# Optimization experiments

Hardware: AMD Instinct MI355X
Metric: run time of the kernel (lower is better)

## Reference

```python
import jax, jax.numpy as jnp
import numpy as np

B, S, H, E = 8, 512, 1024, 8
T = B * S            # total tokens
CAP = T // E         # capacity, capacity_factor = 1.0


def _moe(x, wg, ew1, eb1, ew2, eb2):
    # x: [T, H] tokens; top-1 gating with capacity, DeepSpeed-style dispatch/combine
    gates = jax.nn.softmax(x @ wg)                      # [T, E]
    idx = jnp.argmax(gates, axis=-1)                    # [T]
    mask1 = jax.nn.one_hot(idx, E, dtype=x.dtype)       # [T, E]
    locations = jnp.cumsum(mask1, axis=0) - 1.0         # position within expert queue
    mask1 = mask1 * (locations < CAP).astype(x.dtype)   # drop overflow tokens
    gates1 = jnp.sum(gates * mask1, axis=-1)            # [T] combine weight
    locs = jnp.sum(locations * mask1, axis=-1).astype(jnp.int32)  # [T]
    loc_oh = jax.nn.one_hot(locs, CAP, dtype=x.dtype)   # [T, C]
    combine = gates1[:, None, None] * mask1[:, :, None] * loc_oh[:, None, :]  # [T,E,C]
    dispatch = (combine > 0).astype(x.dtype)            # [T, E, C]
    xd = jnp.einsum('sec,sm->ecm', dispatch, x)         # gather tokens per expert
    h = jnp.einsum('ecm,emn->ecn', xd, ew1) + eb1[:, None, :]
    h = jnp.einsum('ecn,enp->ecp', h, ew2) + eb2[:, None, :]
    return jnp.einsum('sec,ecm->sm', combine, h)        # scatter back, weighted


def setup_inputs() -> dict:
    key = jax.random.key(0)
    ks = jax.random.split(key, 16)
    w = lambda k, shape: jax.random.normal(k, shape, jnp.float32) * 0.02
    return {
        'x': jax.random.normal(ks[0], (B, S, H), jnp.float32),
        'y': jax.random.randint(ks[1], (B,), 0, H),
        'w1': w(ks[2], (H, H)), 'b1': jnp.zeros((H,), jnp.float32),
        'w2': w(ks[3], (H, H)), 'b2': jnp.zeros((H,), jnp.float32),
        'w3': w(ks[4], (H, H)), 'b3': jnp.zeros((H,), jnp.float32),
        'wg1': w(ks[5], (H, E)),
        'e1_w1': w(ks[6], (E, H, H)), 'e1_b1': jnp.zeros((E, H), jnp.float32),
        'e1_w2': w(ks[7], (E, H, H)), 'e1_b2': jnp.zeros((E, H), jnp.float32),
        'wg2': w(ks[8], (H, E)),
        'e2_w1': w(ks[9], (E, H, H)), 'e2_b1': jnp.zeros((E, H), jnp.float32),
        'e2_w2': w(ks[10], (E, H, H)), 'e2_b2': jnp.zeros((E, H), jnp.float32),
    }


def reference(x, y, w1, b1, w2, b2, w3, b3, wg1, e1_w1, e1_b1, e1_w2, e1_b2,
              wg2, e2_w1, e2_b1, e2_w2, e2_b2):
    xf = x.reshape(-1, H)                               # [T, H]
    hidden = xf @ w1 + b1
    out = _moe(hidden, wg1, e1_w1, e1_b1, e1_w2, e1_b2)
    out = out @ w2 + b2
    out = _moe(out, wg2, e2_w1, e2_b1, e2_w2, e2_b2)
    out = out @ w3 + b3
    hidden = hidden + out
    sent = hidden.reshape(B, S, H).mean(axis=1)         # [B, H] logits
    logp = jax.nn.log_softmax(sent, axis=-1)
    return -jnp.mean(logp[jnp.arange(B), y])
```

## Files before the change

kernel.cpp:

```cpp
#include <hip/hip_runtime.h>

#define TOK 4096
#define HID 1024
#define NEXP 8
#define CAP 512
#define WSZ 1048576

typedef _Float16 f16;
typedef f16 f16x8 __attribute__((ext_vector_type(8)));
typedef f16 f16x4 __attribute__((ext_vector_type(4)));
typedef f16 f16x2 __attribute__((ext_vector_type(2)));
typedef float f32x4 __attribute__((ext_vector_type(4)));

typedef const __attribute__((address_space(1))) void gvoid;
typedef __attribute__((address_space(3))) void lvoid;

__device__ __forceinline__ void gld16(const void* g, void* l) {
  __builtin_amdgcn_global_load_lds((gvoid*)g, (lvoid*)l, 16, 0, 0);
}

__device__ __forceinline__ void wtrans(const float* __restrict__ src,
                                       f16* __restrict__ dst,
                                       int nb, int kb0, float* lds, int tid)
{
  const int n = tid >> 3, seg = tid & 7;
  #define WSTAGE(ks, buf)                                                    \
    {                                                                        \
      _Pragma("unroll")                                                      \
      for (int i = 0; i < 2; ++i) {                                          \
        int p = i * 512 + tid;                                               \
        int r = p >> 4, c = p & 15;                                          \
        int cg = c ^ ((r >> 2) & 15);                                        \
        gld16(src + (size_t)(kb0 + (ks) * 64 + r) * HID + nb + cg * 4,       \
              lds + (buf) * 4096 + p * 4);                                   \
      }                                                                      \
    }
  WSTAGE(0, 0);
  #pragma unroll
  for (int s = 0; s < 4; ++s) {
    if (s == 0)      { WSTAGE(1, 1); asm volatile("s_waitcnt vmcnt(2)" ::: "memory"); }
    else if (s == 1) { WSTAGE(2, 0); asm volatile("s_waitcnt vmcnt(3)" ::: "memory"); }
    else if (s == 2) { WSTAGE(3, 1); asm volatile("s_waitcnt vmcnt(3)" ::: "memory"); }
    else             {               asm volatile("s_waitcnt vmcnt(1)" ::: "memory"); }
    asm volatile("s_barrier" ::: "memory");
    const float* B = lds + (s & 1) * 4096;
    f16x8 o;
    #pragma unroll
    for (int j = 0; j < 8; ++j) {
      int r = seg * 8 + j;
      int cl = (n >> 2) ^ ((r >> 2) & 15);
      o[j] = (f16)B[r * 64 + cl * 4 + (n & 3)];
    }
    *(f16x8*)&dst[(size_t)(nb + n) * HID + kb0 + s * 64 + seg * 8] = o;
    asm volatile("s_barrier" ::: "memory");
  }
  #undef WSTAGE
}

template<int MODE>
__global__ __launch_bounds__(512, 4) void gemm_fused(
    const f16* __restrict__ A, const f16* __restrict__ Bt,
    const float* __restrict__ bias, f16* __restrict__ C,
    const int* __restrict__ rowmap, const float* __restrict__ gmax,
    int rowsPerExpert, long bStride, int biasStride,
    const float* __restrict__ tsrc, f16* __restrict__ tdst, int nGemm)
{
  __shared__ __align__(16) unsigned char smem[65536];
  const int tid = threadIdx.x;

  if ((int)blockIdx.x >= nGemm) {
    const int tb = blockIdx.x - nGemm;
    const int mat = tb >> 6, slab = tb & 63;
    wtrans(tsrc + (size_t)mat * WSZ, tdst + (size_t)mat * WSZ,
           (slab & 15) * 64, (slab >> 4) * 256, (float*)smem, tid);
    return;
  }

  f16* As0 = (f16*)smem;
  f16* Bs0 = (f16*)(smem + 32768);
  const int w = tid >> 6, l = tid & 63;
  const int wr = w >> 2, wc = w & 3;

  const int orig = blockIdx.x;
  const int sw = (orig & 7) * 32 + (orig >> 3);
  const int bx = sw & 7, by = sw >> 3;
  const int e = (by * 128) / rowsPerExpert;

  const int lr = l >> 3;
  const int chunkSw = ((l & 7) ^ lr) * 8;

  const f16* pst[4];
  if (w < 4) {
    #pragma unroll
    for (int i = 0; i < 4; ++i) {
      int r = by * 128 + w * 32 + i * 8 + lr;
      long tok = r;
      if (MODE == 1) { int t = rowmap[r]; tok = (t < 0) ? (long)TOK : (long)t; }
      pst[i] = A + tok * HID + chunkSw;
    }
  } else {
    #pragma unroll
    for (int i = 0; i < 4; ++i)
      pst[i] = Bt + (size_t)e * bStride
             + (size_t)(bx * 128 + (w - 4) * 32 + i * 8 + lr) * HID + chunkSw;
  }

  f32x4 acc[4][2];
  #pragma unroll
  for (int i = 0; i < 4; ++i)
    #pragma unroll
    for (int j = 0; j < 2; ++j) acc[i][j] = (f32x4){0.f, 0.f, 0.f, 0.f};

  const int g = l >> 4, c = l & 15, sa = c & 7;

  {
    f16* db = (w < 4) ? As0 + (w * 32) * 64 : Bs0 + ((w - 4) * 32) * 64;
    #pragma unroll
    for (int i = 0; i < 4; ++i) gld16(pst[i], db + i * 8 * 64);
  }

  int cur = 0;
  for (int t = 0; t < 15; ++t) {
    {
      const int k0 = (t + 1) * 64;
      f16* db = (w < 4) ? As0 + ((cur ^ 1) * 8192) + (w * 32) * 64
                        : Bs0 + ((cur ^ 1) * 8192) + ((w - 4) * 32) * 64;
      #pragma unroll
      for (int i = 0; i < 4; ++i) gld16(pst[i] + k0, db + i * 8 * 64);
    }
    asm volatile("s_waitcnt vmcnt(4)" ::: "memory");
    asm volatile("s_barrier" ::: "memory");
    __builtin_amdgcn_s_setprio(1);
    #pragma unroll
    for (int h = 0; h < 2; ++h) {
      const int q = ((h * 4 + g) ^ sa) * 8;
      f16x8 af[4], bf[2];
      #pragma unroll
      for (int mi = 0; mi < 4; ++mi)
        af[mi] = *(const f16x8*)&As0[cur * 8192 + (wr * 64 + mi * 16 + c) * 64 + q];
      #pragma unroll
      for (int ni = 0; ni < 2; ++ni)
        bf[ni] = *(const f16x8*)&Bs0[cur * 8192 + (wc * 32 + ni * 16 + c) * 64 + q];
      #pragma unroll
      for (int mi = 0; mi < 4; ++mi)
        #pragma unroll
        for (int ni = 0; ni < 2; ++ni)
          acc[mi][ni] = __builtin_amdgcn_mfma_f32_16x16x32_f16(
              af[mi], bf[ni], acc[mi][ni], 0, 0, 0);
    }
    __builtin_amdgcn_s_setprio(0);
    asm volatile("s_barrier" ::: "memory");
    cur ^= 1;
  }
  asm volatile("s_waitcnt vmcnt(0)" ::: "memory");
  asm volatile("s_barrier" ::: "memory");
  __builtin_amdgcn_s_setprio(1);
  #pragma unroll
  for (int h = 0; h < 2; ++h) {
    const int q = ((h * 4 + g) ^ sa) * 8;
    f16x8 af[4], bf[2];
    #pragma unroll
    for (int mi = 0; mi < 4; ++mi)
      af[mi] = *(const f16x8*)&As0[cur * 8192 + (wr * 64 + mi * 16 + c) * 64 + q];
    #pragma unroll
    for (int ni = 0; ni < 2; ++ni)
      bf[ni] = *(const f16x8*)&Bs0[cur * 8192 + (wc * 32 + ni * 16 + c) * 64 + q];
    #pragma unroll
    for (int mi = 0; mi < 4; ++mi)
      #pragma unroll
      for (int ni = 0; ni < 2; ++ni)
        acc[mi][ni] = __builtin_amdgcn_mfma_f32_16x16x32_f16(
            af[mi], bf[ni], acc[mi][ni], 0, 0, 0);
  }
  __builtin_amdgcn_s_setprio(0);

  int tk[4][4];
  float gv[4][4];
  if (MODE == 2) {
    #pragma unroll
    for (int mi = 0; mi < 4; ++mi)
      #pragma unroll
      for (int rr = 0; rr < 4; ++rr) {
        int r = by * 128 + wr * 64 + mi * 16 + g * 4 + rr;
        int t = rowmap[r];
        tk[mi][rr] = t;
        gv[mi][rr] = (t >= 0) ? gmax[t] : 0.f;
      }
  }
  #pragma unroll
  for (int ni = 0; ni < 2; ++ni) {
    const int col = bx * 128 + wc * 32 + ni * 16 + c;
    const float bv = bias[(size_t)e * biasStride + col];
    #pragma unroll
    for (int mi = 0; mi < 4; ++mi) {
      #pragma unroll
      for (int rr = 0; rr < 4; ++rr) {
        const float v = acc[mi][ni][rr] + bv;
        if (MODE == 2) {
          if (tk[mi][rr] >= 0)
            C[(size_t)tk[mi][rr] * HID + col] = (f16)(v * gv[mi][rr]);
        } else {
          const int row = by * 128 + wr * 64 + mi * 16 + g * 4 + rr;
          C[(size_t)row * HID + col] = (f16)v;
        }
      }
    }
  }
}

__global__ __launch_bounds__(512) void prep2(
    const float* __restrict__ x, f16* __restrict__ X0,
    f16* __restrict__ c1, f16* __restrict__ c2,
    f16* __restrict__ p1, f16* __restrict__ p2,
    const float* __restrict__ w1, const float* __restrict__ w2,
    const float* __restrict__ w3, f16* __restrict__ WT)
{
  __shared__ __align__(16) float lds[2 * 4096];
  const int tid = threadIdx.x;
  if ((int)blockIdx.x < 1024) {
    const f16x8 zz = {0, 0, 0, 0, 0, 0, 0, 0};
    const size_t i = (size_t)blockIdx.x * 512 + tid;
    #pragma unroll
    for (int it = 0; it < 2; ++it) {
      const size_t idx = i + (size_t)it * 524288;
      float4 v = *(const float4*)&x[idx * 4];
      f16x4 o = {(f16)v.x, (f16)v.y, (f16)v.z, (f16)v.w};
      *(f16x4*)&X0[idx * 4] = o;
    }
    ((f16x8*)c1)[i] = zz;
    ((f16x8*)c2)[i] = zz;
    if (i < 128) { ((f16x8*)p1)[i] = zz; ((f16x8*)p2)[i] = zz; }
    return;
  }
  const int tb = blockIdx.x - 1024;
  const int z = tb >> 6, slab = tb & 63;
  const float* src = (z == 0) ? w1 : (z == 1) ? w2 : w3;
  wtrans(src, WT + (size_t)z * WSZ, (slab & 15) * 64, (slab >> 4) * 256,
         lds, tid);
}

__global__ __launch_bounds__(256) void gate_kernel(
    const f16* __restrict__ act, const float* __restrict__ wg,
    int* __restrict__ idx, float* __restrict__ gmax)
{
  const int tid = threadIdx.x;
  const int tok = blockIdx.x * 8 + (tid >> 5);
  const int sl = tid & 31;
  const f16* row = act + (size_t)tok * HID + sl * 32;
  float xv[32];
  #pragma unroll
  for (int v = 0; v < 4; ++v) {
    f16x8 hv = *(const f16x8*)(row + v * 8);
    #pragma unroll
    for (int j = 0; j < 8; ++j) xv[v * 8 + j] = (float)hv[j];
  }
  float p[NEXP];
  #pragma unroll
  for (int e = 0; e < NEXP; ++e) p[e] = 0.f;
  const float4* w4 = (const float4*)(wg + (size_t)(sl * 32) * NEXP);
  #pragma unroll
  for (int j = 0; j < 32; ++j) {
    float4 lo = w4[2 * j], hi = w4[2 * j + 1];
    p[0] += xv[j] * lo.x; p[1] += xv[j] * lo.y;
    p[2] += xv[j] * lo.z; p[3] += xv[j] * lo.w;
    p[4] += xv[j] * hi.x; p[5] += xv[j] * hi.y;
    p[6] += xv[j] * hi.z; p[7] += xv[j] * hi.w;
  }
  #pragma unroll
  for (int m = 1; m < 32; m <<= 1) {
    #pragma unroll
    for (int e = 0; e < NEXP; ++e) p[e] += __shfl_xor(p[e], m, 64);
  }
  if (sl == 0) {
    float mx = p[0]; int am = 0;
    #pragma unroll
    for (int e = 1; e < NEXP; ++e)
      if (p[e] > mx) { mx = p[e]; am = e; }
    float s = 0.f;
    #pragma unroll
    for (int e = 0; e < NEXP; ++e) s += expf(p[e] - mx);
    idx[tok] = am;
    gmax[tok] = 1.f / s;
  }
}

__global__ __launch_bounds__(512) void scan_kernel(
    const int* __restrict__ idx, int* __restrict__ rowmap)
{
  __shared__ int sidx[TOK];
  const int tid = threadIdx.x;
  for (int i = tid; i < TOK; i += 512) sidx[i] = idx[i];
  for (int i = tid; i < NEXP * CAP; i += 512) rowmap[i] = -1;
  __syncthreads();
  const int wave = tid >> 6, lane = tid & 63;
  int running = 0;
  for (int ch = 0; ch < TOK / 64; ++ch) {
    int t = ch * 64 + lane;
    bool flag = (sidx[t] == wave);
    unsigned long long m = __ballot(flag);
    int pos = running + __popcll(m & ((1ull << lane) - 1ull));
    if (flag && pos < CAP) rowmap[wave * CAP + pos] = t;
    running += __popcll(m);
  }
}

__global__ __launch_bounds__(256) void meanHC_kernel(
    const f16* __restrict__ Hb, const f16* __restrict__ C2b,
    float* __restrict__ pH, float* __restrict__ pC)
{
  const int h2 = blockIdx.x * 256 + threadIdx.x;
  const int b = blockIdx.y, sc = blockIdx.z;
  const f16x2* pa = (const f16x2*)(Hb + ((size_t)b * 512 + sc * 32) * HID) + h2;
  const f16x2* pc = (const f16x2*)(C2b + ((size_t)b * 512 + sc * 32) * HID) + h2;
  float a0 = 0.f, a1 = 0.f, c0 = 0.f, c1 = 0.f;
  #pragma unroll 4
  for (int s = 0; s < 32; ++s) {
    f16x2 va = pa[(size_t)s * 512];
    f16x2 vc = pc[(size_t)s * 512];
    a0 += (float)va[0]; a1 += (float)va[1];
    c0 += (float)vc[0]; c1 += (float)vc[1];
  }
  float* oh = pH + ((size_t)sc * 8 + b) * HID;
  float* oc = pC + ((size_t)sc * 8 + b) * HID;
  oh[h2 * 2] = a0; oh[h2 * 2 + 1] = a1;
  oc[h2 * 2] = c0; oc[h2 * 2 + 1] = c1;
}

__global__ __launch_bounds__(256) void sent_kernel(
    const float* __restrict__ pH, const float* __restrict__ pC,
    const f16* __restrict__ WT2, const float* __restrict__ b3,
    float* __restrict__ sent)
{
  __shared__ float c2m[HID];
  const int tid = threadIdx.x;
  const int b = blockIdx.x >> 2, ch = blockIdx.x & 3;
  for (int kk = tid; kk < HID; kk += 256) {
    float s = 0.f;
    #pragma unroll
    for (int sc = 0; sc < 16; ++sc) s += pC[((size_t)sc * 8 + b) * HID + kk];
    c2m[kk] = s * (1.f / 512.f);
  }
  __syncthreads();
  const int col = ch * 256 + tid;
  float hv = 0.f;
  #pragma unroll
  for (int sc = 0; sc < 16; ++sc) hv += pH[((size_t)sc * 8 + b) * HID + col];
  float acc = hv * (1.f / 512.f) + b3[col];
  const f16* wrow = WT2 + (size_t)col * HID;
  for (int k0 = 0; k0 < HID; k0 += 8) {
    f16x8 wv = *(const f16x8*)(wrow + k0);
    #pragma unroll
    for (int j = 0; j < 8; ++j) acc += c2m[k0 + j] * (float)wv[j];
  }
  sent[b * HID + col] = acc;
}

__global__ __launch_bounds__(1024) void loss_kernel(
    const float* __restrict__ sent, const int* __restrict__ y,
    float* __restrict__ out)
{
  __shared__ float red[17];
  const int tid = threadIdx.x;
  const int wid = tid >> 6, lane = tid & 63;
  float loss = 0.0f;
  for (int b = 0; b < 8; ++b) {
    const float v = sent[b * HID + tid];
    float m = v;
    #pragma unroll
    for (int o = 32; o; o >>= 1) m = fmaxf(m, __shfl_xor(m, o, 64));
    if (lane == 0) red[wid] = m;
    __syncthreads();
    if (tid < 16) {
      float mm = red[tid];
      #pragma unroll
      for (int o = 8; o; o >>= 1) mm = fmaxf(mm, __shfl_xor(mm, o, 16));
      if (tid == 0) red[16] = mm;
    }
    __syncthreads();
    const float M = red[16];
    float s = expf(v - M);
    #pragma unroll
    for (int o = 32; o; o >>= 1) s += __shfl_xor(s, o, 64);
    __syncthreads();
    if (lane == 0) red[wid] = s;
    __syncthreads();
    if (tid < 16) {
      float ss = red[tid];
      #pragma unroll
      for (int o = 8; o; o >>= 1) ss += __shfl_xor(ss, o, 16);
      if (tid == 0) red[16] = M + logf(ss);
    }
    __syncthreads();
    if (tid == 0) loss += -(sent[b * HID + y[b]] - red[16]);
    __syncthreads();
  }
  if (tid == 0) out[0] = loss * (1.0f / 8.0f);
}

extern "C" void kernel_launch(void* const* d_in, const int* in_sizes, int n_in,
                              void* d_out, int out_size, void* d_ws, size_t ws_size,
                              hipStream_t stream)
{
  const float* x    = (const float*)d_in[0];
  const int*   y    = (const int*)d_in[1];
  const float* w1   = (const float*)d_in[2];
  const float* b1   = (const float*)d_in[3];
  const float* w2   = (const float*)d_in[4];
  const float* b2   = (const float*)d_in[5];
  const float* w3   = (const float*)d_in[6];
  const float* b3   = (const float*)d_in[7];
  const float* wg1  = (const float*)d_in[8];
  const float* e1w1 = (const float*)d_in[9];
  const float* e1b1 = (const float*)d_in[10];
  const float* e1w2 = (const float*)d_in[11];
  const float* e1b2 = (const float*)d_in[12];
  const float* wg2  = (const float*)d_in[13];
  const float* e2w1 = (const float*)d_in[14];
  const float* e2b1 = (const float*)d_in[15];
  const float* e2w2 = (const float*)d_in[16];
  const float* e2b2 = (const float*)d_in[17];

  f16* WT = (f16*)d_ws;
  f16* X0 = WT + (size_t)35 * WSZ;
  f16* H  = X0 + (size_t)TOK * HID;
  f16* EA = H + (size_t)(TOK + 1) * HID;
  f16* C1 = EA + (size_t)TOK * HID;
  f16* M1 = C1 + (size_t)TOK * HID;
  f16* C2 = M1 + (size_t)(TOK + 1) * HID;
  float* gmax  = (float*)(C2 + (size_t)TOK * HID);
  int* idx     = (int*)(gmax + TOK);
  int* rowmap  = idx + TOK;
  float* sent  = (float*)(rowmap + NEXP * CAP);
  float* pH    = sent + 8 * HID;
  float* pC    = pH + 16 * 8 * HID;

  f16* WTe1a = WT + (size_t)3 * WSZ;
  f16* WTe1b = WT + (size_t)11 * WSZ;
  f16* WTe2a = WT + (size_t)19 * WSZ;
  f16* WTe2b = WT + (size_t)27 * WSZ;

  const int FUSED = 256 + 512;

  prep2<<<1216, 512, 0, stream>>>(x, X0, C1, C2,
                                  H + (size_t)TOK * HID, M1 + (size_t)TOK * HID,
                                  w1, w2, w3, WT);

  gemm_fused<0><<<FUSED, 512, 0, stream>>>(X0, WT, b1, H, nullptr, nullptr,
                                           TOK, 0, 0, e1w1, WTe1a, 256);

  gate_kernel<<<512, 256, 0, stream>>>(H, wg1, idx, gmax);
  scan_kernel<<<1, 512, 0, stream>>>(idx, rowmap);
  gemm_fused<1><<<FUSED, 512, 0, stream>>>(H, WTe1a, e1b1, EA, rowmap, nullptr,
                                           CAP, WSZ, HID, e1w2, WTe1b, 256);
  gemm_fused<2><<<FUSED, 512, 0, stream>>>(EA, WTe1b, e1b2, C1, rowmap, gmax,
                                           CAP, WSZ, HID, e2w1, WTe2a, 256);

  gemm_fused<0><<<FUSED, 512, 0, stream>>>(C1, WT + (size_t)1 * WSZ, b2, M1,
                                           nullptr, nullptr, TOK, 0, 0,
                                           e2w2, WTe2b, 256);

  gate_kernel<<<512, 256, 0, stream>>>(M1, wg2, idx, gmax);
  scan_kernel<<<1, 512, 0, stream>>>(idx, rowmap);
  gemm_fused<1><<<256, 512, 0, stream>>>(M1, WTe2a, e2b1, EA, rowmap, nullptr,
                                         CAP, WSZ, HID, w1, WT, 256);
  gemm_fused<2><<<256, 512, 0, stream>>>(EA, WTe2b, e2b2, C2, rowmap, gmax,
                                         CAP, WSZ, HID, w1, WT, 256);

  meanHC_kernel<<<dim3(2, 8, 16), 256, 0, stream>>>(H, C2, pH, pC);
  sent_kernel<<<32, 256, 0, stream>>>(pH, pC, WT + (size_t)2 * WSZ, b3, sent);
  loss_kernel<<<1, 1024, 0, stream>>>(sent, y, (float*)d_out);
}
```

Measured before the change: 216.0 us.

## Fold gate projection into preceding linear layer and compute gating alongside GEMM

Precomputes G = W·Wg and Gb = b·Wg in the prep kernel so gating logits can be computed directly from the GEMM input rather than its output. The gate computation is then run as extra blocks inside the same gemm_fused launch, removing the separate gate_kernel launches and the serial dependency on the layer output. This changes fp rounding, since the logits are computed in a different order from f16 inputs, which could flip argmax decisions on near-ties. It also adds extra blocks to each fused launch.

Result: slower. 244.8 us (+13.3%).

```diff
diff --git a/kernel.cpp b/kernel.cpp
--- a/kernel.cpp
+++ b/kernel.cpp
@@ -63,10 +63,58 @@
     const float* __restrict__ bias, f16* __restrict__ C,
     const int* __restrict__ rowmap, const float* __restrict__ gmax,
     int rowsPerExpert, long bStride, int biasStride,
-    const float* __restrict__ tsrc, f16* __restrict__ tdst, int nGemm)
+    const float* __restrict__ tsrc, f16* __restrict__ tdst,
+    const f16* __restrict__ gX, const float* __restrict__ G,
+    const float* __restrict__ Gb, int* __restrict__ gidx,
+    float* __restrict__ ggmax, int nGemm, int nTrans)
 {
   __shared__ __align__(16) unsigned char smem[65536];
   const int tid = threadIdx.x;
+
+  if ((int)blockIdx.x >= nGemm + nTrans) {
+    const int gb = blockIdx.x - nGemm - nTrans;
+    const int tok = gb * 16 + (tid >> 5);
+    const int sl = tid & 31;
+    const f16* row = gX + (size_t)tok * HID + sl * 32;
+    float xv[32];
+    #pragma unroll
+    for (int v = 0; v < 4; ++v) {
+      f16x8 hv = *(const f16x8*)(row + v * 8);
+      #pragma unroll
+      for (int j = 0; j < 8; ++j) xv[v * 8 + j] = (float)hv[j];
+    }
+    float p[NEXP];
+    #pragma unroll
+    for (int e = 0; e < NEXP; ++e) p[e] = 0.f;
+    const float4* g4 = (const float4*)(G + (size_t)(sl * 32) * NEXP);
+    #pragma unroll
+    for (int j = 0; j < 32; ++j) {
+      float4 lo = g4[2 * j], hi = g4[2 * j + 1];
+      p[0] += xv[j] * lo.x; p[1] += xv[j] * lo.y;
+      p[2] += xv[j] * lo.z; p[3] += xv[j] * lo.w;
+      p[4] += xv[j] * hi.x; p[5] += xv[j] * hi.y;
+      p[6] += xv[j] * hi.z; p[7] += xv[j] * hi.w;
+    }
+    #pragma unroll
+    for (int m = 1; m < 32; m <<= 1) {
+      #pragma unroll
+      for (int e = 0; e < NEXP; ++e) p[e] += __shfl_xor(p[e], m, 64);
+    }
+    if (sl == 0) {
+      #pragma unroll
+      for (int e = 0; e < NEXP; ++e) p[e] += Gb[e];
+      float mx = p[0]; int am = 0;
+      #pragma unroll
+      for (int e = 1; e < NEXP; ++e)
+        if (p[e] > mx) { mx = p[e]; am = e; }
+      float s = 0.f;
+      #pragma unroll
+      for (int e = 0; e < NEXP; ++e) s += expf(p[e] - mx);
+      gidx[tok] = am;
+      ggmax[tok] = 1.f / s;
+    }
+    return;
+  }
 
   if ((int)blockIdx.x >= nGemm) {
     const int tb = blockIdx.x - nGemm;
@@ -213,7 +261,11 @@
     f16* __restrict__ c1, f16* __restrict__ c2,
     f16* __restrict__ p1, f16* __restrict__ p2,
     const float* __restrict__ w1, const float* __restrict__ w2,
-    const float* __restrict__ w3, f16* __restrict__ WT)
+    const float* __restrict__ w3, f16* __restrict__ WT,
+    const float* __restrict__ wg1, const float* __restrict__ wg2,
+    const float* __restrict__ b1, const float* __restrict__ b2,
+    float* __restrict__ G1, float* __restrict__ G2,
+    float* __restrict__ Gb1, float* __restrict__ Gb2)
 {
   __shared__ __align__(16) float lds[2 * 4096];
   const int tid = threadIdx.x;
@@ -232,55 +284,37 @@
     if (i < 128) { ((f16x8*)p1)[i] = zz; ((f16x8*)p2)[i] = zz; }
     return;
   }
-  const int tb = blockIdx.x - 1024;
-  const int z = tb >> 6, slab = tb & 63;
-  const float* src = (z == 0) ? w1 : (z == 1) ? w2 : w3;
-  wtrans(src, WT + (size_t)z * WSZ, (slab & 15) * 64, (slab >> 4) * 256,
-         lds, tid);
-}
-
-__global__ __launch_bounds__(256) void gate_kernel(
-    const f16* __restrict__ act, const float* __restrict__ wg,
-    int* __restrict__ idx, float* __restrict__ gmax)
-{
-  const int tid = threadIdx.x;
-  const int tok = blockIdx.x * 8 + (tid >> 5);
-  const int sl = tid & 31;
-  const f16* row = act + (size_t)tok * HID + sl * 32;
-  float xv[32];
-  #pragma unroll
-  for (int v = 0; v < 4; ++v) {
-    f16x8 hv = *(const f16x8*)(row + v * 8);
-    #pragma unroll
-    for (int j = 0; j < 8; ++j) xv[v * 8 + j] = (float)hv[j];
-  }
-  float p[NEXP];
-  #pragma unroll
-  for (int e = 0; e < NEXP; ++e) p[e] = 0.f;
-  const float4* w4 = (const float4*)(wg + (size_t)(sl * 32) * NEXP);
-  #pragma unroll
-  for (int j = 0; j < 32; ++j) {
-    float4 lo = w4[2 * j], hi = w4[2 * j + 1];
-    p[0] += xv[j] * lo.x; p[1] += xv[j] * lo.y;
-    p[2] += xv[j] * lo.z; p[3] += xv[j] * lo.w;
-    p[4] += xv[j] * hi.x; p[5] += xv[j] * hi.y;
-    p[6] += xv[j] * hi.z; p[7] += xv[j] * hi.w;
-  }
-  #pragma unroll
-  for (int m = 1; m < 32; m <<= 1) {
-    #pragma unroll
-    for (int e = 0; e < NEXP; ++e) p[e] += __shfl_xor(p[e], m, 64);
-  }
-  if (sl == 0) {
-    float mx = p[0]; int am = 0;
-    #pragma unroll
-    for (int e = 1; e < NEXP; ++e)
-      if (p[e] > mx) { mx = p[e]; am = e; }
+  if ((int)blockIdx.x < 1216) {
+    const int tb = blockIdx.x - 1024;
+    const int z = tb >> 6, slab = tb & 63;
+    const float* src = (z == 0) ? w1 : (z == 1) ? w2 : w3;
+    wtrans(src, WT + (size_t)z * WSZ, (slab & 15) * 64, (slab >> 4) * 256,
+           lds, tid);
+    return;
+  }
+  const int gz = blockIdx.x - 1216;
+  const int which = gz >> 4;
+  const int kb = (gz & 15) * 64;
+  const float* w   = which ? w2 : w1;
+  const float* wgp = which ? wg2 : wg1;
+  const float* b   = which ? b2 : b1;
+  float* Gout  = which ? G2 : G1;
+  float* GbOut = which ? Gb2 : Gb1;
+  for (int i = tid; i < 8192; i += 512) lds[i] = wgp[i];
+  __syncthreads();
+  const int k = kb + (tid >> 3), ee = tid & 7;
+  const float4* wrow = (const float4*)(w + (size_t)k * HID);
+  float acc = 0.f;
+  for (int m4 = 0; m4 < 256; ++m4) {
+    float4 wv = wrow[m4];
+    acc += wv.x * lds[(m4 * 4 + 0) * 8 + ee] + wv.y * lds[(m4 * 4 + 1) * 8 + ee]
+         + wv.z * lds[(m4 * 4 + 2) * 8 + ee] + wv.w * lds[(m4 * 4 + 3) * 8 + ee];
+  }
+  Gout[k * 8 + ee] = acc;
+  if (kb == 0 && tid < 8) {
     float s = 0.f;
-    #pragma unroll
-    for (int e = 0; e < NEXP; ++e) s += expf(p[e] - mx);
-    idx[tok] = am;
-    gmax[tok] = 1.f / s;
+    for (int m = 0; m < HID; ++m) s += b[m] * lds[m * 8 + tid];
+    GbOut[tid] = s;
   }
 }
 
@@ -430,7 +464,11 @@
   float* gmax  = (float*)(C2 + (size_t)TOK * HID);
   int* idx     = (int*)(gmax + TOK);
   int* rowmap  = idx + TOK;
-  float* sent  = (float*)(rowmap + NEXP * CAP);
+  float* G1    = (float*)(rowmap + NEXP * CAP);
+  float* G2    = G1 + HID * NEXP;
+  float* Gb1   = G2 + HID * NEXP;
+  float* Gb2   = Gb1 + 8;
+  float* sent  = Gb2 + 8;
   float* pH    = sent + 8 * HID;
   float* pC    = pH + 16 * 8 * HID;
 
@@ -439,32 +477,34 @@
   f16* WTe2a = WT + (size_t)19 * WSZ;
   f16* WTe2b = WT + (size_t)27 * WSZ;
 
-  const int FUSED = 256 + 512;
-
-  prep2<<<1216, 512, 0, stream>>>(x, X0, C1, C2,
+  prep2<<<1248, 512, 0, stream>>>(x, X0, C1, C2,
                                   H + (size_t)TOK * HID, M1 + (size_t)TOK * HID,
-                                  w1, w2, w3, WT);
-
-  gemm_fused<0><<<FUSED, 512, 0, stream>>>(X0, WT, b1, H, nullptr, nullptr,
-                                           TOK, 0, 0, e1w1, WTe1a, 256);
-
-  gate_kernel<<<512, 256, 0, stream>>>(H, wg1, idx, gmax);
+                                  w1, w2, w3, WT, wg1, wg2, b1, b2,
+                                  G1, G2, Gb1, Gb2);
+
+  gemm_fused<0><<<256 + 512 + 256, 512, 0, stream>>>(
+      X0, WT, b1, H, nullptr, nullptr, TOK, 0, 0,
+      e1w1, WTe1a, X0, G1, Gb1, idx, gmax, 256, 512);
+
   scan_kernel<<<1, 512, 0, stream>>>(idx, rowmap);
-  gemm_fused<1><<<FUSED, 512, 0, stream>>>(H, WTe1a, e1b1, EA, rowmap, nullptr,
-                                           CAP, WSZ, HID, e1w2, WTe1b, 256);
-  gemm_fused<2><<<FUSED, 512, 0, stream>>>(EA, WTe1b, e1b2, C1, rowmap, gmax,
-                                           CAP, WSZ, HID, e2w1, WTe2a, 256);
-
-  gemm_fused<0><<<FUSED, 512, 0, stream>>>(C1, WT + (size_t)1 * WSZ, b2, M1,
-                                           nullptr, nullptr, TOK, 0, 0,
-                                           e2w2, WTe2b, 256);
-
-  gate_kernel<<<512, 256, 0, stream>>>(M1, wg2, idx, gmax);
+  gemm_fused<1><<<256 + 512, 512, 0, stream>>>(
+      H, WTe1a, e1b1, EA, rowmap, nullptr, CAP, WSZ, HID,
+      e1w2, WTe1b, nullptr, nullptr, nullptr, nullptr, nullptr, 256, 512);
+  gemm_fused<2><<<256 + 512, 512, 0, stream>>>(
+      EA, WTe1b, e1b2, C1, rowmap, gmax, CAP, WSZ, HID,
+      e2w1, WTe2a, nullptr, nullptr, nullptr, nullptr, nullptr, 256, 512);
+
+  gemm_fused<0><<<256 + 512 + 256, 512, 0, stream>>>(
+      C1, WT + (size_t)1 * WSZ, b2, M1, nullptr, nullptr, TOK, 0, 0,
+      e2w2, WTe2b, C1, G2, Gb2, idx, gmax, 256, 512);
+
   scan_kernel<<<1, 512, 0, stream>>>(idx, rowmap);
-  gemm_fused<1><<<256, 512, 0, stream>>>(M1, WTe2a, e2b1, EA, rowmap, nullptr,
-                                         CAP, WSZ, HID, w1, WT, 256);
-  gemm_fused<2><<<256, 512, 0, stream>>>(EA, WTe2b, e2b2, C2, rowmap, gmax,
-                                         CAP, WSZ, HID, w1, WT, 256);
+  gemm_fused<1><<<256, 512, 0, stream>>>(
+      M1, WTe2a, e2b1, EA, rowmap, nullptr, CAP, WSZ, HID,
+      nullptr, nullptr, nullptr, nullptr, nullptr, nullptr, nullptr, 256, 0);
+  gemm_fused<2><<<256, 512, 0, stream>>>(
+      EA, WTe2b, e2b2, C2, rowmap, gmax, CAP, WSZ, HID,
+      nullptr, nullptr, nullptr, nullptr, nullptr, nullptr, nullptr, 256, 0);
 
   meanHC_kernel<<<dim3(2, 8, 16), 256, 0, stream>>>(H, C2, pH, pC);
   sent_kernel<<<32, 256, 0, stream>>>(pH, pC, WT + (size_t)2 * WSZ, b3, sent);
```
